# Performance work log

Hardware: AMD Instinct MI355X
Metric: run time of the kernel (lower is better)

Reference implementation:

```python
import jax, jax.numpy as jnp
import numpy as np

H = W = 256          # input_img_height (square images)
N_NODES = 8          # camera graph nodes
N_EDGES = 64         # ~fully connected directed graph
FEAT = 1024          # edge_feat_dim
BN_EPS = 1e-5


def setup_inputs() -> dict:
    key = jax.random.key(0)
    ks = jax.random.split(key, 8)
    d = {}
    d["x"] = jax.random.normal(ks[0], (N_NODES, 3 * H * W), dtype=jnp.float32)
    d["edge_index"] = jax.random.randint(ks[1], (2, N_EDGES), 0, N_NODES)
    # ResNet stem params (conv1 replaced to take 6 channels)
    d["conv1_w"] = jax.random.normal(ks[2], (64, 6, 7, 7), dtype=jnp.float32) * 0.05
    d["bn_gamma"] = jnp.ones((64,), jnp.float32)
    d["bn_beta"] = jnp.zeros((64,), jnp.float32)
    d["bn_mean"] = jnp.zeros((64,), jnp.float32)
    d["bn_var"] = jnp.ones((64,), jnp.float32)
    d["fc_w"] = jax.random.normal(ks[3], (FEAT, 64), dtype=jnp.float32) * 0.05
    d["fc_b"] = jnp.zeros((FEAT,), jnp.float32)
    d["fc_xyz_w"] = jax.random.normal(ks[4], (3, FEAT), dtype=jnp.float32) * 0.05
    d["fc_xyz_b"] = jnp.zeros((3,), jnp.float32)
    d["fc_wpqr_w"] = jax.random.normal(ks[5], (3, FEAT), dtype=jnp.float32) * 0.05
    d["fc_wpqr_b"] = jnp.zeros((3,), jnp.float32)
    return d


def _edge_extractor(ef, conv1_w, bn_gamma, bn_beta, bn_mean, bn_var, fc_w, fc_b):
    # conv1: 6->64, 7x7, stride 2, pad 3, no bias
    y = jax.lax.conv_general_dilated(
        ef, conv1_w, window_strides=(2, 2), padding=[(3, 3), (3, 3)],
        dimension_numbers=("NCHW", "OIHW", "NCHW"))
    # BatchNorm (inference form with running stats), fused scale/shift
    scale = (bn_gamma * jax.lax.rsqrt(bn_var + BN_EPS))[None, :, None, None]
    shift = (bn_beta - bn_mean * bn_gamma * jax.lax.rsqrt(bn_var + BN_EPS))[None, :, None, None]
    y = jax.nn.relu(y * scale + shift)
    # maxpool 3x3 stride 2 pad 1
    y = jax.lax.reduce_window(y, -jnp.inf, jax.lax.max,
                              (1, 1, 3, 3), (1, 1, 2, 2),
                              [(0, 0), (0, 0), (1, 1), (1, 1)])
    # AdaptiveAvgPool2d(1) + fc to edge_feat_dim
    y = jnp.mean(y, axis=(2, 3))                     # [E, 64]
    return y @ fc_w.T + fc_b                         # [E, FEAT]


def reference(x, edge_index, conv1_w, bn_gamma, bn_beta, bn_mean, bn_var,
              fc_w, fc_b, fc_xyz_w, fc_xyz_b, fc_wpqr_w, fc_wpqr_b):
    imgs = x.reshape(N_NODES, 3, H, W)
    # compute_edge_features, vectorized: gather min/max node per edge, concat channels
    nmin = jnp.min(edge_index, axis=0)               # [E]
    nmax = jnp.max(edge_index, axis=0)               # [E]
    edge_feat = jnp.concatenate([imgs[nmin], imgs[nmax]], axis=1)  # [E, 6, H, W]
    ef = _edge_extractor(edge_feat, conv1_w, bn_gamma, bn_beta, bn_mean, bn_var, fc_w, fc_b)
    ef = jax.nn.relu(ef)
    # droprate == 0 -> no dropout
    xyz = ef @ fc_xyz_w.T + fc_xyz_b                 # [E, 3]
    wpqr = ef @ fc_wpqr_w.T + fc_wpqr_b              # [E, 3]
    full = jnp.concatenate([xyz, wpqr], axis=1)      # [E, 6]
    return (full[:N_NODES], full)
```

## Files before the change

### kernel.cpp

```cpp
#include <hip/hip_runtime.h>
#include <hip/hip_bf16.h>

#define N_NODES 8
#define N_EDGES 64
#define CO 64
#define OH 128
#define OW 128
#define FEAT 1024
#define BN_EPS 1e-5f

#define OFF_PARTIAL 0
#define OFF_XPAD    151552
#define OFF_WB      3471616
#define OFF_A       3520768
#define OFF_B       20297984
#define OFF_FCWT    37075200

#define RS_W 136
#define XROW 132

typedef short bf16x8 __attribute__((ext_vector_type(8)));
typedef float f32x4  __attribute__((ext_vector_type(4)));

__device__ __forceinline__ unsigned short f2bf(float f) {
    unsigned u = __float_as_uint(f);
    u += 0x7fffu + ((u >> 16) & 1u);
    return (unsigned short)(u >> 16);
}
__device__ __forceinline__ float blo(unsigned u) { return __uint_as_float(u << 16); }
__device__ __forceinline__ float bhi(unsigned u) { return __uint_as_float(u & 0xffff0000u); }

__global__ __launch_bounds__(256) void prep_kernel(
        const float* __restrict__ x, const float* __restrict__ w,
        const float* __restrict__ gamma, const float* __restrict__ var,
        const float* __restrict__ fc_w,
        unsigned* __restrict__ xpad, unsigned short* __restrict__ wb2,
        float* __restrict__ fc_wT) {
    int idx = blockIdx.x * 256 + threadIdx.x;
    if (idx < 8 * 3 * 262 * XROW) {
        int u   = idx % XROW;
        int r   = idx / XROW;
        int iyp = r % 262;
        int nc  = r / 262;
        int iy  = iyp - 3;
        unsigned val = 0u;
        if ((unsigned)iy < 256u) {
            int c0 = 2 * u - 3;
            const float* row = x + (size_t)nc * 65536 + iy * 256;
            float f0 = ((unsigned)c0 < 256u) ? row[c0] : 0.f;
            float f1 = ((unsigned)(c0 + 1) < 256u) ? row[c0 + 1] : 0.f;
            val = (unsigned)f2bf(f0) | ((unsigned)f2bf(f1) << 16);
        }
        xpad[idx] = val;
    }
    if (idx < 2 * 64 * 192) {
        int tp = idx % 192;
        int c  = (idx / 192) & 63;
        int h  = idx / (192 * 64);
        int rr = tp >> 3, kx = tp & 7;
        float val = 0.f;
        if (rr < 21 && kx < 7) {
            int ci = rr / 7, ky = rr % 7;
            float sc = gamma[c] * rsqrtf(var[c] + BN_EPS);
            val = w[((c * 6 + h * 3 + ci) * 7 + ky) * 7 + kx] * sc;
        }
        wb2[(rr * 128 + h * 64 + c) * 8 + kx] = f2bf(val);
    }
    if (idx < CO * FEAT) {
        int c = idx >> 10, f = idx & 1023;
        fc_wT[idx] = fc_w[f * CO + c];
    }
}

__global__ __launch_bounds__(256, 3) void conv_kernel(
        const unsigned* __restrict__ xpad, const unsigned short* __restrict__ wb2,
        const float* __restrict__ gamma, const float* __restrict__ beta,
        const float* __restrict__ mean,  const float* __restrict__ var,
        unsigned short* __restrict__ A2, unsigned short* __restrict__ B2) {
    int bx  = blockIdx.x;
    int r16 = bx & 7;
    int idx = bx >> 3;
    int n   = idx >> 4;
    int oy  = (r16 << 4) + (idx & 15);
    int t   = threadIdx.x;

    __shared__ __align__(16) char smem[32768];
    unsigned* rawu = (unsigned*)smem;

    const unsigned* src = xpad + (size_t)n * (3 * 262 * XROW);
    for (int k = t; k < 816; k += 256) {
        int g  = k % 34;
        int rr = k / 34;
        uint4 v = make_uint4(0u, 0u, 0u, 0u);
        if (rr < 21 && g < 33) {
            int ci = (rr * 147) >> 10;
            int ky = rr - ci * 7;
            v = *(const uint4*)(src + (ci * 262 + 2 * oy + ky) * XROW + 4 * g);
        }
        *(uint4*)&rawu[rr * RS_W + 4 * g] = v;
    }
    __syncthreads();

    int wv = t >> 6, lane = t & 63;
    int hg = wv >> 1;
    int wg = wv & 1;
    int quad = lane >> 4, m = lane & 15;

    f32x4 acc[4][4];
#pragma unroll
    for (int ct = 0; ct < 4; ++ct)
#pragma unroll
        for (int nt = 0; nt < 4; ++nt)
            acc[ct][nt] = (f32x4){0.f, 0.f, 0.f, 0.f};

    const bf16x8* wbv = (const bf16x8*)wb2;

#pragma unroll 2
    for (int s = 0; s < 6; ++s) {
        int rq = 4 * s + quad;
        bf16x8 afrag[4];
#pragma unroll
        for (int nt = 0; nt < 4; ++nt) {
            int ox = 64 * wg + 16 * nt + m;
            int base = rq * RS_W + ox;
            union { unsigned u[4]; bf16x8 v; } bb;
            bb.u[0] = rawu[base];     bb.u[1] = rawu[base + 1];
            bb.u[2] = rawu[base + 2]; bb.u[3] = rawu[base + 3];
            afrag[nt] = bb.v;
        }
#pragma unroll
        for (int ct = 0; ct < 4; ++ct) {
            bf16x8 wfrag = wbv[rq * 128 + hg * 64 + 16 * ct + m];
#pragma unroll
            for (int nt = 0; nt < 4; ++nt)
                acc[ct][nt] = __builtin_amdgcn_mfma_f32_16x16x32_bf16(
                                  afrag[nt], wfrag, acc[ct][nt], 0, 0, 0);
        }
    }

    float sh[4] = {0.f, 0.f, 0.f, 0.f};
    if (hg) {
#pragma unroll
        for (int ct = 0; ct < 4; ++ct) {
            int c = 16 * ct + m;
            float sc = gamma[c] * rsqrtf(var[c] + BN_EPS);
            sh[ct] = beta[c] - mean[c] * sc;
        }
    }

    __syncthreads();
    unsigned short* T = (unsigned short*)smem;

#pragma unroll
    for (int ct = 0; ct < 4; ++ct) {
        int chp = hg * 64 + 16 * ct + m;
        int sw  = (chp & 7) << 2;
#pragma unroll
        for (int nt = 0; nt < 4; ++nt) {
            int px0 = 64 * wg + 16 * nt + 4 * quad;
            float v0 = acc[ct][nt][0] + sh[ct];
            float v1 = acc[ct][nt][1] + sh[ct];
            float v2 = acc[ct][nt][2] + sh[ct];
            float v3 = acc[ct][nt][3] + sh[ct];
            uint2 pk;
            pk.x = (unsigned)f2bf(v0) | ((unsigned)f2bf(v1) << 16);
            pk.y = (unsigned)f2bf(v2) | ((unsigned)f2bf(v3) << 16);
            int gs = ((px0 >> 2) ^ sw);
            *(uint2*)&T[chp * 128 + gs * 4] = pk;
        }
    }
    __syncthreads();

#pragma unroll
    for (int rr = 0; rr < 4; ++rr) {
        int row = rr * 32 + (t >> 3), slot = t & 7;
        int hh = row >> 6, ch = row & 63;
        int swr = (row & 7) << 2;
        unsigned short* dst = (hh ? B2 : A2)
                            + ((size_t)(n * CO + ch) << 14) + (oy << 7) + slot * 16;
#pragma unroll
        for (int i = 0; i < 2; ++i) {
            int g  = slot * 4 + i * 2;
            int gs = g ^ swr;
            *(uint4*)(dst + i * 8) = *(uint4*)&T[row * 128 + gs * 4];
        }
    }
}

__global__ __launch_bounds__(256, 4) void pool_kernel(
        const unsigned short* __restrict__ A2,
        const unsigned short* __restrict__ B2,
        float* __restrict__ partial) {
    int pb  = blockIdx.x;
    int xcd = pb & 7;
    int q   = pb >> 3;
    int c   = q >> 1;
    int rt  = xcd * 2 + (q & 1);
    int t   = threadIdx.x;

    __shared__ unsigned short S[2 * 8 * 9 * 128];

    for (int k = t; k < 2304; k += 256) {
        int slot = k & 15;
        int r    = (k >> 4) % 9;
        int tn   = (k >> 4) / 9;
        int grow = 8 * rt - 1 + r;
        uint4 v = make_uint4(0u, 0u, 0u, 0u);
        if (grow >= 0) {
            const unsigned short* src = (tn >= 8) ? B2 : A2;
            int node = tn & 7;
            v = *(const uint4*)(src + ((size_t)(node * CO + c) << 14)
                                    + (grow << 7) + slot * 8);
        }
        *(uint4*)&S[tn * 1152 + (r << 7) + slot * 8] = v;
    }
    __syncthreads();

    int wv = t >> 6, lane = t & 63;
    int esub = lane >> 4, tc = lane & 15;

    for (int i = 0; i < 3; ++i) {
        int sidx = 12 * wv + 4 * i + esub;
        bool valid = sidx < 36;
        int ss = valid ? sidx : 0;
        int pi = 0, rem = ss;
        while (rem >= 8 - pi) { rem -= 8 - pi; ++pi; }
        int pj = pi + rem;
        const unsigned short* pa  = &S[pi * 1152];
        const unsigned short* pb2 = &S[(8 + pj) * 1152];

        float mx[4][4];
#pragma unroll
        for (int p = 0; p < 4; ++p)
#pragma unroll
            for (int qq = 0; qq < 4; ++qq) mx[p][qq] = 0.f;

#pragma unroll
        for (int r = 0; r < 9; ++r) {
            uint4 ga = *(const uint4*)(pa + (r << 7) + tc * 8);
            uint4 gb = *(const uint4*)(pb2 + (r << 7) + tc * 8);
            float ha = 0.f, hb = 0.f;
            if (tc > 0) {
                ha = bhi(*(const unsigned*)(pa + (r << 7) + tc * 8 - 2));
                hb = bhi(*(const unsigned*)(pb2 + (r << 7) + tc * 8 - 2));
            }
            float z0 = ha + hb;
            float z1 = blo(ga.x) + blo(gb.x), z2 = bhi(ga.x) + bhi(gb.x);
            float z3 = blo(ga.y) + blo(gb.y), z4 = bhi(ga.y) + bhi(gb.y);
            float z5 = blo(ga.z) + blo(gb.z), z6 = bhi(ga.z) + bhi(gb.z);
            float z7 = blo(ga.w) + blo(gb.w), z8 = bhi(ga.w) + bhi(gb.w);
            float h0 = fmaxf(fmaxf(z0, z1), z2);
            float h1 = fmaxf(fmaxf(z2, z3), z4);
            float h2 = fmaxf(fmaxf(z4, z5), z6);
            float h3 = fmaxf(fmaxf(z6, z7), z8);
            if (r & 1) {
                int p = (r - 1) >> 1;
                mx[p][0] = fmaxf(mx[p][0], h0); mx[p][1] = fmaxf(mx[p][1], h1);
                mx[p][2] = fmaxf(mx[p][2], h2); mx[p][3] = fmaxf(mx[p][3], h3);
            } else {
                if (r >= 2) {
                    int p = (r >> 1) - 1;
                    mx[p][0] = fmaxf(mx[p][0], h0); mx[p][1] = fmaxf(mx[p][1], h1);
                    mx[p][2] = fmaxf(mx[p][2], h2); mx[p][3] = fmaxf(mx[p][3], h3);
                }
                if (r <= 6) {
                    int p = r >> 1;
                    mx[p][0] = fmaxf(mx[p][0], h0); mx[p][1] = fmaxf(mx[p][1], h1);
                    mx[p][2] = fmaxf(mx[p][2], h2); mx[p][3] = fmaxf(mx[p][3], h3);
                }
            }
        }

        float sum = 0.f;
#pragma unroll
        for (int p = 0; p < 4; ++p)
#pragma unroll
            for (int qq = 0; qq < 4; ++qq) sum += fmaxf(mx[p][qq], 0.f);

        sum += __shfl_down(sum, 8, 64);
        sum += __shfl_down(sum, 4, 64);
        sum += __shfl_down(sum, 2, 64);
        sum += __shfl_down(sum, 1, 64);
        if (tc == 0 && valid)
            partial[(rt * 36 + sidx) * 64 + c] = sum;
    }
}

__global__ __launch_bounds__(1024) void head_kernel(
        const int* __restrict__ ei, const float* __restrict__ partial,
        const float* __restrict__ fc_wT,  const float* __restrict__ fc_b,
        const float* __restrict__ xyz_w,  const float* __restrict__ xyz_b,
        const float* __restrict__ wpqr_w, const float* __restrict__ wpqr_b,
        float* __restrict__ out) {
    int e = blockIdx.x;
    int t = threadIdx.x;
    int a0 = ei[e], a1 = ei[N_EDGES + e];
    int pi = min(a0, a1), pj = max(a0, a1);
    int rank = pi * 8 - ((pi * (pi + 1)) >> 1) + pj;
    __shared__ float pl[CO];
    if (t < CO) {
        float s = 0.f;
#pragma unroll
        for (int rt = 0; rt < 16; ++rt)
            s += partial[(rt * 36 + rank) * 64 + t];
        pl[t] = s * (1.f / 4096.f);
    }
    __syncthreads();

    float d = fc_b[t];
#pragma unroll
    for (int c = 0; c < CO; ++c)
        d = fmaf(pl[c], fc_wT[c * FEAT + t], d);
    d = fmaxf(d, 0.f);

    float s[6];
#pragma unroll
    for (int r = 0; r < 3; ++r) {
        s[r]     = d * xyz_w[r * FEAT + t];
        s[3 + r] = d * wpqr_w[r * FEAT + t];
    }
#pragma unroll
    for (int r = 0; r < 6; ++r)
#pragma unroll
        for (int off = 32; off > 0; off >>= 1)
            s[r] += __shfl_down(s[r], off, 64);

    __shared__ float red[16][6];
    if ((t & 63) == 0) {
#pragma unroll
        for (int r = 0; r < 6; ++r) red[t >> 6][r] = s[r];
    }
    __syncthreads();
    if (t < 6) {
        float v = 0.f;
#pragma unroll
        for (int w = 0; w < 16; ++w) v += red[w][t];
        v += (t < 3) ? xyz_b[t] : wpqr_b[t - 3];
        out[48 + e * 6 + t] = v;
        if (e < 8) out[e * 6 + t] = v;
    }
}

extern "C" void kernel_launch(void* const* d_in, const int* in_sizes, int n_in,
                              void* d_out, int out_size, void* d_ws, size_t ws_size,
                              hipStream_t stream) {
    const float* x        = (const float*)d_in[0];
    const int*   ei       = (const int*)d_in[1];
    const float* conv1_w  = (const float*)d_in[2];
    const float* bn_gamma = (const float*)d_in[3];
    const float* bn_beta  = (const float*)d_in[4];
    const float* bn_mean  = (const float*)d_in[5];
    const float* bn_var   = (const float*)d_in[6];
    const float* fc_w     = (const float*)d_in[7];
    const float* fc_b     = (const float*)d_in[8];
    const float* xyz_w    = (const float*)d_in[9];
    const float* xyz_b    = (const float*)d_in[10];
    const float* wpqr_w   = (const float*)d_in[11];
    const float* wpqr_b   = (const float*)d_in[12];
    float* out = (float*)d_out;

    char* ws = (char*)d_ws;
    float*          partial = (float*)(ws + OFF_PARTIAL);
    unsigned*       xpad    = (unsigned*)(ws + OFF_XPAD);
    unsigned short* wb2     = (unsigned short*)(ws + OFF_WB);
    unsigned short* A2      = (unsigned short*)(ws + OFF_A);
    unsigned short* B2      = (unsigned short*)(ws + OFF_B);
    float*          fc_wT   = (float*)(ws + OFF_FCWT);

    int img_work = 8 * 3 * 262 * XROW;
    prep_kernel<<<(img_work + 255) / 256, 256, 0, stream>>>(
        x, conv1_w, bn_gamma, bn_var, fc_w, xpad, wb2, fc_wT);
    conv_kernel<<<1024, 256, 0, stream>>>(xpad, wb2, bn_gamma, bn_beta,
                                          bn_mean, bn_var, A2, B2);
    pool_kernel<<<1024, 256, 0, stream>>>(A2, B2, partial);
    head_kernel<<<64, 1024, 0, stream>>>(ei, partial, fc_wT, fc_b,
                                         xyz_w, xyz_b, wpqr_w, wpqr_b, out);
}
```

Before: 119.4 us.

## Fuse image padding/bf16 conversion into conv load and fc transpose into pool

Removes the padded bf16 image staging buffer. The conv kernel now reads fp32 input directly, doing padding and bf16 packing in its shared-memory load loop. The fc weight transpose moves into the pool kernel, so the prep kernel shrinks to the small weight-prep work. The pool kernel grows to 576 threads so each of its 9 waves handles exactly 4 of the 36 pair slots in one pass instead of looping three times. The aim is to cut a full read/write pass over the images and prep launch cost, at the price of scalar strided fp32 global loads in conv and a larger block in pool.

```diff
diff --git a/kernel.cpp b/kernel.cpp
--- a/kernel.cpp
+++ b/kernel.cpp
@@ -10,14 +10,12 @@
 #define BN_EPS 1e-5f
 
 #define OFF_PARTIAL 0
-#define OFF_XPAD    151552
 #define OFF_WB      3471616
 #define OFF_A       3520768
 #define OFF_B       20297984
 #define OFF_FCWT    37075200
 
 #define RS_W 136
-#define XROW 132
 
 typedef short bf16x8 __attribute__((ext_vector_type(8)));
 typedef float f32x4  __attribute__((ext_vector_type(4)));
@@ -31,28 +29,10 @@
 __device__ __forceinline__ float bhi(unsigned u) { return __uint_as_float(u & 0xffff0000u); }
 
 __global__ __launch_bounds__(256) void prep_kernel(
-        const float* __restrict__ x, const float* __restrict__ w,
+        const float* __restrict__ w,
         const float* __restrict__ gamma, const float* __restrict__ var,
-        const float* __restrict__ fc_w,
-        unsigned* __restrict__ xpad, unsigned short* __restrict__ wb2,
-        float* __restrict__ fc_wT) {
+        unsigned short* __restrict__ wb2) {
     int idx = blockIdx.x * 256 + threadIdx.x;
-    if (idx < 8 * 3 * 262 * XROW) {
-        int u   = idx % XROW;
-        int r   = idx / XROW;
-        int iyp = r % 262;
-        int nc  = r / 262;
-        int iy  = iyp - 3;
-        unsigned val = 0u;
-        if ((unsigned)iy < 256u) {
-            int c0 = 2 * u - 3;
-            const float* row = x + (size_t)nc * 65536 + iy * 256;
-            float f0 = ((unsigned)c0 < 256u) ? row[c0] : 0.f;
-            float f1 = ((unsigned)(c0 + 1) < 256u) ? row[c0 + 1] : 0.f;
-            val = (unsigned)f2bf(f0) | ((unsigned)f2bf(f1) << 16);
-        }
-        xpad[idx] = val;
-    }
     if (idx < 2 * 64 * 192) {
         int tp = idx % 192;
         int c  = (idx / 192) & 63;
@@ -66,14 +46,10 @@
         }
         wb2[(rr * 128 + h * 64 + c) * 8 + kx] = f2bf(val);
     }
-    if (idx < CO * FEAT) {
-        int c = idx >> 10, f = idx & 1023;
-        fc_wT[idx] = fc_w[f * CO + c];
-    }
 }
 
 __global__ __launch_bounds__(256, 3) void conv_kernel(
-        const unsigned* __restrict__ xpad, const unsigned short* __restrict__ wb2,
+        const float* __restrict__ x, const unsigned short* __restrict__ wb2,
         const float* __restrict__ gamma, const float* __restrict__ beta,
         const float* __restrict__ mean,  const float* __restrict__ var,
         unsigned short* __restrict__ A2, unsigned short* __restrict__ B2) {
@@ -87,7 +63,7 @@
     __shared__ __align__(16) char smem[32768];
     unsigned* rawu = (unsigned*)smem;
 
-    const unsigned* src = xpad + (size_t)n * (3 * 262 * XROW);
+    const float* xn = x + (size_t)n * (3 * 65536);
     for (int k = t; k < 816; k += 256) {
         int g  = k % 34;
         int rr = k / 34;
@@ -95,7 +71,23 @@
         if (rr < 21 && g < 33) {
             int ci = (rr * 147) >> 10;
             int ky = rr - ci * 7;
-            v = *(const uint4*)(src + (ci * 262 + 2 * oy + ky) * XROW + 4 * g);
+            int iy = 2 * oy + ky - 3;
+            if ((unsigned)iy < 256u) {
+                const float* row = xn + ci * 65536 + iy * 256;
+                int c0 = 8 * g - 3;
+                float f[8];
+#pragma unroll
+                for (int j = 0; j < 8; ++j) {
+                    int c  = c0 + j;
+                    int cc = min(max(c, 0), 255);
+                    float fv = row[cc];
+                    f[j] = (c == cc) ? fv : 0.f;
+                }
+                v.x = (unsigned)f2bf(f[0]) | ((unsigned)f2bf(f[1]) << 16);
+                v.y = (unsigned)f2bf(f[2]) | ((unsigned)f2bf(f[3]) << 16);
+                v.z = (unsigned)f2bf(f[4]) | ((unsigned)f2bf(f[5]) << 16);
+                v.w = (unsigned)f2bf(f[6]) | ((unsigned)f2bf(f[7]) << 16);
+            }
         }
         *(uint4*)&rawu[rr * RS_W + 4 * g] = v;
     }
@@ -187,10 +179,11 @@
     }
 }
 
-__global__ __launch_bounds__(256, 4) void pool_kernel(
+__global__ __launch_bounds__(576) void pool_kernel(
         const unsigned short* __restrict__ A2,
         const unsigned short* __restrict__ B2,
-        float* __restrict__ partial) {
+        const float* __restrict__ fc_w,
+        float* __restrict__ partial, float* __restrict__ fc_wT) {
     int pb  = blockIdx.x;
     int xcd = pb & 7;
     int q   = pb >> 3;
@@ -198,9 +191,15 @@
     int rt  = xcd * 2 + (q & 1);
     int t   = threadIdx.x;
 
+    if (t < 64) {
+        int idx = pb * 64 + t;
+        int cc = idx >> 10, f = idx & 1023;
+        fc_wT[idx] = fc_w[f * CO + cc];
+    }
+
     __shared__ unsigned short S[2 * 8 * 9 * 128];
 
-    for (int k = t; k < 2304; k += 256) {
+    for (int k = t; k < 2304; k += 576) {
         int slot = k & 15;
         int r    = (k >> 4) % 9;
         int tn   = (k >> 4) / 9;
@@ -219,71 +218,67 @@
     int wv = t >> 6, lane = t & 63;
     int esub = lane >> 4, tc = lane & 15;
 
-    for (int i = 0; i < 3; ++i) {
-        int sidx = 12 * wv + 4 * i + esub;
-        bool valid = sidx < 36;
-        int ss = valid ? sidx : 0;
-        int pi = 0, rem = ss;
-        while (rem >= 8 - pi) { rem -= 8 - pi; ++pi; }
-        int pj = pi + rem;
-        const unsigned short* pa  = &S[pi * 1152];
-        const unsigned short* pb2 = &S[(8 + pj) * 1152];
-
-        float mx[4][4];
-#pragma unroll
-        for (int p = 0; p < 4; ++p)
-#pragma unroll
-            for (int qq = 0; qq < 4; ++qq) mx[p][qq] = 0.f;
-
-#pragma unroll
-        for (int r = 0; r < 9; ++r) {
-            uint4 ga = *(const uint4*)(pa + (r << 7) + tc * 8);
-            uint4 gb = *(const uint4*)(pb2 + (r << 7) + tc * 8);
-            float ha = 0.f, hb = 0.f;
-            if (tc > 0) {
-                ha = bhi(*(const unsigned*)(pa + (r << 7) + tc * 8 - 2));
-                hb = bhi(*(const unsigned*)(pb2 + (r << 7) + tc * 8 - 2));
-            }
-            float z0 = ha + hb;
-            float z1 = blo(ga.x) + blo(gb.x), z2 = bhi(ga.x) + bhi(gb.x);
-            float z3 = blo(ga.y) + blo(gb.y), z4 = bhi(ga.y) + bhi(gb.y);
-            float z5 = blo(ga.z) + blo(gb.z), z6 = bhi(ga.z) + bhi(gb.z);
-            float z7 = blo(ga.w) + blo(gb.w), z8 = bhi(ga.w) + bhi(gb.w);
-            float h0 = fmaxf(fmaxf(z0, z1), z2);
-            float h1 = fmaxf(fmaxf(z2, z3), z4);
-            float h2 = fmaxf(fmaxf(z4, z5), z6);
-            float h3 = fmaxf(fmaxf(z6, z7), z8);
-            if (r & 1) {
-                int p = (r - 1) >> 1;
+    int sidx = 4 * wv + esub;
+    int pi = 0, rem = sidx;
+    while (rem >= 8 - pi) { rem -= 8 - pi; ++pi; }
+    int pj = pi + rem;
+    const unsigned short* pa  = &S[pi * 1152];
+    const unsigned short* pb2 = &S[(8 + pj) * 1152];
+
+    float mx[4][4];
+#pragma unroll
+    for (int p = 0; p < 4; ++p)
+#pragma unroll
+        for (int qq = 0; qq < 4; ++qq) mx[p][qq] = 0.f;
+
+#pragma unroll
+    for (int r = 0; r < 9; ++r) {
+        uint4 ga = *(const uint4*)(pa + (r << 7) + tc * 8);
+        uint4 gb = *(const uint4*)(pb2 + (r << 7) + tc * 8);
+        float ha = 0.f, hb = 0.f;
+        if (tc > 0) {
+            ha = bhi(*(const unsigned*)(pa + (r << 7) + tc * 8 - 2));
+            hb = bhi(*(const unsigned*)(pb2 + (r << 7) + tc * 8 - 2));
+        }
+        float z0 = ha + hb;
+        float z1 = blo(ga.x) + blo(gb.x), z2 = bhi(ga.x) + bhi(gb.x);
+        float z3 = blo(ga.y) + blo(gb.y), z4 = bhi(ga.y) + bhi(gb.y);
+        float z5 = blo(ga.z) + blo(gb.z), z6 = bhi(ga.z) + bhi(gb.z);
+        float z7 = blo(ga.w) + blo(gb.w), z8 = bhi(ga.w) + bhi(gb.w);
+        float h0 = fmaxf(fmaxf(z0, z1), z2);
+        float h1 = fmaxf(fmaxf(z2, z3), z4);
+        float h2 = fmaxf(fmaxf(z4, z5), z6);
+        float h3 = fmaxf(fmaxf(z6, z7), z8);
+        if (r & 1) {
+            int p = (r - 1) >> 1;
+            mx[p][0] = fmaxf(mx[p][0], h0); mx[p][1] = fmaxf(mx[p][1], h1);
+            mx[p][2] = fmaxf(mx[p][2], h2); mx[p][3] = fmaxf(mx[p][3], h3);
+        } else {
+            if (r >= 2) {
+                int p = (r >> 1) - 1;
                 mx[p][0] = fmaxf(mx[p][0], h0); mx[p][1] = fmaxf(mx[p][1], h1);
                 mx[p][2] = fmaxf(mx[p][2], h2); mx[p][3] = fmaxf(mx[p][3], h3);
-            } else {
-                if (r >= 2) {
-                    int p = (r >> 1) - 1;
-                    mx[p][0] = fmaxf(mx[p][0], h0); mx[p][1] = fmaxf(mx[p][1], h1);
-                    mx[p][2] = fmaxf(mx[p][2], h2); mx[p][3] = fmaxf(mx[p][3], h3);
-                }
-                if (r <= 6) {
-                    int p = r >> 1;
-                    mx[p][0] = fmaxf(mx[p][0], h0); mx[p][1] = fmaxf(mx[p][1], h1);
-                    mx[p][2] = fmaxf(mx[p][2], h2); mx[p][3] = fmaxf(mx[p][3], h3);
-                }
             }
-        }
-
-        float sum = 0.f;
-#pragma unroll
-        for (int p = 0; p < 4; ++p)
-#pragma unroll
-            for (int qq = 0; qq < 4; ++qq) sum += fmaxf(mx[p][qq], 0.f);
-
-        sum += __shfl_down(sum, 8, 64);
-        sum += __shfl_down(sum, 4, 64);
-        sum += __shfl_down(sum, 2, 64);
-        sum += __shfl_down(sum, 1, 64);
-        if (tc == 0 && valid)
-            partial[(rt * 36 + sidx) * 64 + c] = sum;
-    }
+            if (r <= 6) {
+                int p = r >> 1;
+                mx[p][0] = fmaxf(mx[p][0], h0); mx[p][1] = fmaxf(mx[p][1], h1);
+                mx[p][2] = fmaxf(mx[p][2], h2); mx[p][3] = fmaxf(mx[p][3], h3);
+            }
+        }
+    }
+
+    float sum = 0.f;
+#pragma unroll
+    for (int p = 0; p < 4; ++p)
+#pragma unroll
+        for (int qq = 0; qq < 4; ++qq) sum += fmaxf(mx[p][qq], 0.f);
+
+    sum += __shfl_down(sum, 8, 64);
+    sum += __shfl_down(sum, 4, 64);
+    sum += __shfl_down(sum, 2, 64);
+    sum += __shfl_down(sum, 1, 64);
+    if (tc == 0)
+        partial[(rt * 36 + sidx) * 64 + c] = sum;
 }
 
 __global__ __launch_bounds__(1024) void head_kernel(
@@ -361,18 +356,15 @@
 
     char* ws = (char*)d_ws;
     float*          partial = (float*)(ws + OFF_PARTIAL);
-    unsigned*       xpad    = (unsigned*)(ws + OFF_XPAD);
     unsigned short* wb2     = (unsigned short*)(ws + OFF_WB);
     unsigned short* A2      = (unsigned short*)(ws + OFF_A);
     unsigned short* B2      = (unsigned short*)(ws + OFF_B);
     float*          fc_wT   = (float*)(ws + OFF_FCWT);
 
-    int img_work = 8 * 3 * 262 * XROW;
-    prep_kernel<<<(img_work + 255) / 256, 256, 0, stream>>>(
-        x, conv1_w, bn_gamma, bn_var, fc_w, xpad, wb2, fc_wT);
-    conv_kernel<<<1024, 256, 0, stream>>>(xpad, wb2, bn_gamma, bn_beta,
+    prep_kernel<<<96, 256, 0, stream>>>(conv1_w, bn_gamma, bn_var, wb2);
+    conv_kernel<<<1024, 256, 0, stream>>>(x, wb2, bn_gamma, bn_beta,
                                           bn_mean, bn_var, A2, B2);
-    pool_kernel<<<1024, 256, 0, stream>>>(A2, B2, partial);
+    pool_kernel<<<1024, 576, 0, stream>>>(A2, B2, fc_w, partial, fc_wT);
     head_kernel<<<64, 1024, 0, stream>>>(ei, partial, fc_wT, fc_b,
                                          xyz_w, xyz_b, wpqr_w, wpqr_b, out);
 }
```

Measured after the change: 130.3 us. +9.2%, slower.

## Fuse image padding and bf16 conversion into conv kernel staging

Applied to the files above, without the earlier changes.

Removes the separate pass that wrote a padded bf16 copy of the input images to workspace. The conv kernel now reads fp32 rows directly with float4 loads, converts them to bf16 and writes them into shared memory, zeroing the padding columns and rows itself. The weight layout shifts kx by one to match the new one-word left offset. This drops a full image read/write round trip and shrinks the prep launch, in exchange for redundant fp32 loads and conversions across conv blocks that share input rows.

```diff
diff --git a/kernel.cpp b/kernel.cpp
--- a/kernel.cpp
+++ b/kernel.cpp
@@ -10,14 +10,12 @@
 #define BN_EPS 1e-5f
 
 #define OFF_PARTIAL 0
-#define OFF_XPAD    151552
 #define OFF_WB      3471616
 #define OFF_A       3520768
 #define OFF_B       20297984
 #define OFF_FCWT    37075200
 
 #define RS_W 136
-#define XROW 132
 
 typedef short bf16x8 __attribute__((ext_vector_type(8)));
 typedef float f32x4  __attribute__((ext_vector_type(4)));
@@ -31,38 +29,21 @@
 __device__ __forceinline__ float bhi(unsigned u) { return __uint_as_float(u & 0xffff0000u); }
 
 __global__ __launch_bounds__(256) void prep_kernel(
-        const float* __restrict__ x, const float* __restrict__ w,
+        const float* __restrict__ w,
         const float* __restrict__ gamma, const float* __restrict__ var,
         const float* __restrict__ fc_w,
-        unsigned* __restrict__ xpad, unsigned short* __restrict__ wb2,
-        float* __restrict__ fc_wT) {
+        unsigned short* __restrict__ wb2, float* __restrict__ fc_wT) {
     int idx = blockIdx.x * 256 + threadIdx.x;
-    if (idx < 8 * 3 * 262 * XROW) {
-        int u   = idx % XROW;
-        int r   = idx / XROW;
-        int iyp = r % 262;
-        int nc  = r / 262;
-        int iy  = iyp - 3;
-        unsigned val = 0u;
-        if ((unsigned)iy < 256u) {
-            int c0 = 2 * u - 3;
-            const float* row = x + (size_t)nc * 65536 + iy * 256;
-            float f0 = ((unsigned)c0 < 256u) ? row[c0] : 0.f;
-            float f1 = ((unsigned)(c0 + 1) < 256u) ? row[c0 + 1] : 0.f;
-            val = (unsigned)f2bf(f0) | ((unsigned)f2bf(f1) << 16);
-        }
-        xpad[idx] = val;
-    }
     if (idx < 2 * 64 * 192) {
         int tp = idx % 192;
         int c  = (idx / 192) & 63;
         int h  = idx / (192 * 64);
         int rr = tp >> 3, kx = tp & 7;
         float val = 0.f;
-        if (rr < 21 && kx < 7) {
+        if (rr < 21 && kx >= 1) {
             int ci = rr / 7, ky = rr % 7;
             float sc = gamma[c] * rsqrtf(var[c] + BN_EPS);
-            val = w[((c * 6 + h * 3 + ci) * 7 + ky) * 7 + kx] * sc;
+            val = w[((c * 6 + h * 3 + ci) * 7 + ky) * 7 + (kx - 1)] * sc;
         }
         wb2[(rr * 128 + h * 64 + c) * 8 + kx] = f2bf(val);
     }
@@ -73,7 +54,7 @@
 }
 
 __global__ __launch_bounds__(256, 3) void conv_kernel(
-        const unsigned* __restrict__ xpad, const unsigned short* __restrict__ wb2,
+        const float* __restrict__ x, const unsigned short* __restrict__ wb2,
         const float* __restrict__ gamma, const float* __restrict__ beta,
         const float* __restrict__ mean,  const float* __restrict__ var,
         unsigned short* __restrict__ A2, unsigned short* __restrict__ B2) {
@@ -87,17 +68,29 @@
     __shared__ __align__(16) char smem[32768];
     unsigned* rawu = (unsigned*)smem;
 
-    const unsigned* src = xpad + (size_t)n * (3 * 262 * XROW);
-    for (int k = t; k < 816; k += 256) {
-        int g  = k % 34;
-        int rr = k / 34;
-        uint4 v = make_uint4(0u, 0u, 0u, 0u);
-        if (rr < 21 && g < 33) {
-            int ci = (rr * 147) >> 10;
-            int ky = rr - ci * 7;
-            v = *(const uint4*)(src + (ci * 262 + 2 * oy + ky) * XROW + 4 * g);
-        }
-        *(uint4*)&rawu[rr * RS_W + 4 * g] = v;
+    if (t < 168) {
+        int rr = t >> 3, wsel = t & 7;
+        int u = (wsel < 2) ? wsel : (128 + wsel);
+        rawu[rr * RS_W + u] = 0u;
+    } else if (t < 270) {
+        int k2 = t - 168;
+        int rr = 21 + k2 / 34, g = k2 % 34;
+        *(uint4*)&rawu[rr * RS_W + 4 * g] = make_uint4(0u, 0u, 0u, 0u);
+    }
+
+    const float* xn = x + (size_t)n * (3 * 65536);
+    for (int k = t; k < 1344; k += 256) {
+        int rr = k >> 6, q = k & 63;
+        int ci = (rr * 147) >> 10;
+        int ky = rr - ci * 7;
+        int iy = 2 * oy + ky - 3;
+        uint2 pk = make_uint2(0u, 0u);
+        if ((unsigned)iy < 256u) {
+            float4 f = *(const float4*)(xn + ci * 65536 + iy * 256 + 4 * q);
+            pk.x = (unsigned)f2bf(f.x) | ((unsigned)f2bf(f.y) << 16);
+            pk.y = (unsigned)f2bf(f.z) | ((unsigned)f2bf(f.w) << 16);
+        }
+        *(uint2*)&rawu[rr * RS_W + 2 * q + 2] = pk;
     }
     __syncthreads();
 
@@ -361,16 +354,14 @@
 
     char* ws = (char*)d_ws;
     float*          partial = (float*)(ws + OFF_PARTIAL);
-    unsigned*       xpad    = (unsigned*)(ws + OFF_XPAD);
     unsigned short* wb2     = (unsigned short*)(ws + OFF_WB);
     unsigned short* A2      = (unsigned short*)(ws + OFF_A);
     unsigned short* B2      = (unsigned short*)(ws + OFF_B);
     float*          fc_wT   = (float*)(ws + OFF_FCWT);
 
-    int img_work = 8 * 3 * 262 * XROW;
-    prep_kernel<<<(img_work + 255) / 256, 256, 0, stream>>>(
-        x, conv1_w, bn_gamma, bn_var, fc_w, xpad, wb2, fc_wT);
-    conv_kernel<<<1024, 256, 0, stream>>>(xpad, wb2, bn_gamma, bn_beta,
+    prep_kernel<<<256, 256, 0, stream>>>(conv1_w, bn_gamma, bn_var,
+                                         fc_w, wb2, fc_wT);
+    conv_kernel<<<1024, 256, 0, stream>>>(x, wb2, bn_gamma, bn_beta,
                                           bn_mean, bn_var, A2, B2);
     pool_kernel<<<1024, 256, 0, stream>>>(A2, B2, partial);
     head_kernel<<<64, 1024, 0, stream>>>(ei, partial, fc_wT, fc_b,
```

Result: no change. 119.3 us, median of 2 (-0.0%).
